# Kernel optimization log

Hardware: AMD Instinct MI355X
Metric: run time of the kernel (lower is better)

## Reference

```python
import jax, jax.numpy as jnp
import numpy as np
from jax import lax

B, L, D, H, OM = 16, 512, 2048, 512, 5


def _lstm(seq, wih, whh, bih, bhh):
    # seq: [T, B, F]; PyTorch gate order i, f, g, o
    Hh = whh.shape[1]
    Bb = seq.shape[1]
    def step(carry, xt):
        h, c = carry
        g = xt @ wih.T + h @ whh.T + bih + bhh
        i, f, gg, o = jnp.split(g, 4, axis=-1)
        c = jax.nn.sigmoid(f) * c + jax.nn.sigmoid(i) * jnp.tanh(gg)
        h = jax.nn.sigmoid(o) * jnp.tanh(c)
        return (h, c), h
    z = jnp.zeros((Bb, Hh), seq.dtype)
    _, hs = lax.scan(step, (z, z), seq)
    return hs  # [T, B, Hh]


def setup_inputs() -> dict:
    key = jax.random.key(0)
    ks = jax.random.split(key, 17)
    s = 0.02
    f32 = jnp.float32
    inp = {
        "x": jax.random.normal(ks[0], (B, L, D), f32),
        "wb": jax.random.normal(ks[1], (H, D, OM), f32) * s,
        "bb": jax.random.normal(ks[2], (H,), f32) * s,
        "wa": jax.random.normal(ks[3], (H, D, OM), f32) * s,
        "ba": jax.random.normal(ks[4], (H,), f32) * s,
        "wr": jax.random.normal(ks[5], (H, D, 2 * OM), f32) * s,
        "br": jax.random.normal(ks[6], (H,), f32) * s,
        "wih_f": jax.random.normal(ks[7], (4 * H, H + 1), f32) * s,
        "whh_f": jax.random.normal(ks[8], (4 * H, H), f32) * s,
        "bih_f": jax.random.normal(ks[9], (4 * H,), f32) * s,
        "bhh_f": jax.random.normal(ks[10], (4 * H,), f32) * s,
        "wih_r": jax.random.normal(ks[11], (4 * H, H + 1), f32) * s,
        "whh_r": jax.random.normal(ks[12], (4 * H, H), f32) * s,
        "bih_r": jax.random.normal(ks[13], (4 * H,), f32) * s,
        "bhh_r": jax.random.normal(ks[14], (4 * H,), f32) * s,
        "wfc": jax.random.normal(ks[15], (1, 2 * H), f32) * s,
        "bfc": jax.random.normal(ks[16], (1,), f32) * s,
    }
    return inp


def reference(x, wb, bb, wa, ba, wr, br, wih_f, whh_f, bih_f, bhh_f,
              wih_r, whh_r, bih_r, bhh_r, wfc, bfc):
    om = OM
    xc = jnp.transpose(x, (0, 2, 1))  # [B, D, L]
    conv = lambda w, b: lax.conv_general_dilated(
        xc, w, (1,), 'VALID', dimension_numbers=('NCH', 'OIH', 'NCH')) + b[None, :, None]
    cb = conv(wb, bb)  # [B, H, L-om+1]
    ca = conv(wa, ba)  # [B, H, L-om+1]
    cr = conv(wr, br)  # [B, H, L-2om+1]
    T = x.shape[1] - 2 * om  # number of centers c in [om, L-om)
    d_before = cb[:, :, 0:T]          # window [c-om, c) == conv output c-om
    d_after = ca[:, :, om:om + T]     # window [c, c+om) == conv output c
    vts_d = jnp.sum(d_before * d_after, axis=1, keepdims=True)  # [B, 1, T]
    vts_r = cr[:, :, 0:T]             # full window; pool over length-1 is identity
    vts_seq = jnp.concatenate([vts_r, vts_d], axis=1)  # [B, H+1, T]
    seq = jnp.transpose(vts_seq, (2, 0, 1))  # [T, B, H+1]
    hs_f = _lstm(seq, wih_f, whh_f, bih_f, bhh_f)
    hs_r = _lstm(seq[::-1], wih_r, whh_r, bih_r, bhh_r)[::-1]
    h = jnp.concatenate([hs_f, hs_r], axis=-1)  # [T, B, 2H]
    logits = jnp.einsum('tbh,h->tb', h, wfc[0]) + bfc[0]
    return jax.nn.sigmoid(jnp.transpose(logits))  # [B, T]
```

## Files before the change

### kernel.cpp

```cpp
#include <hip/hip_runtime.h>
#include <hip/hip_bf16.h>

typedef short v8s __attribute__((ext_vector_type(8)));
typedef float v4f __attribute__((ext_vector_type(4)));
typedef unsigned int u32;
typedef unsigned short u16;
typedef unsigned long long u64;

__device__ __forceinline__ u16 f2bf(float f) {
    union { float f; u32 u; } x; x.f = f;
    u32 r = x.u + 0x7fffu + ((x.u >> 16) & 1u);
    return (u16)(r >> 16);
}
__device__ __forceinline__ float bf2f(u16 s) {
    union { u32 u; float f; } x; x.u = ((u32)s) << 16;
    return x.f;
}
__device__ __forceinline__ float sigmoidf_(float x) { return 1.f / (1.f + __expf(-x)); }
__device__ __forceinline__ float tanh_fast(float x) {
    float t = fminf(fmaxf(x, -15.f), 15.f);
    float e = __expf(2.f * t);
    return (e - 1.f) / (e + 1.f);
}

__global__ __launch_bounds__(256) void xbf_kernel(const float* __restrict__ x, u16* __restrict__ xbf, int n) {
    int i = (blockIdx.x * 256 + threadIdx.x) * 4;
    if (i + 3 < n) {
        float4 v = *(const float4*)(x + i);
        u16* d = xbf + i;
        d[0] = f2bf(v.x); d[1] = f2bf(v.y); d[2] = f2bf(v.z); d[3] = f2bf(v.w);
    }
}

__global__ __launch_bounds__(256) void packw_kernel(const float* __restrict__ wb, const float* __restrict__ wa,
                                                    const float* __restrict__ wr, u16* __restrict__ W1, u16* __restrict__ W2) {
    long idx = (long)blockIdx.x * 256 + threadIdx.x;
    int which = idx >= (1024L * 10240) ? 1 : 0;
    long rem = idx - (long)which * 1024 * 10240;
    int n = (int)(rem / 10240);
    int kap = (int)(rem % 10240);
    int tap = kap >> 11, d = kap & 2047;
    float v;
    if (n < 512) v = which ? wa[(long)n * 10240 + d * 5 + tap] : wb[(long)n * 10240 + d * 5 + tap];
    else         v = wr[(long)(n - 512) * 20480 + d * 10 + tap + (which ? 5 : 0)];
    (which ? W2 : W1)[rem] = f2bf(v);
}

__global__ __launch_bounds__(256) void packwih_kernel(const float* __restrict__ wf, const float* __restrict__ wr,
                                                      u16* __restrict__ Bp) {
    int idx = blockIdx.x * 256 + threadIdx.x;
    int n = idx / 576, kap = idx % 576;
    int dir = n >> 11, g = n & 2047;
    const float* src = dir ? wr : wf;
    float v = (kap < 513) ? src[(long)g * 513 + kap] : 0.f;
    Bp[idx] = f2bf(v);
}

__global__ __launch_bounds__(256) void packwhh_kernel(const float* __restrict__ whf, const float* __restrict__ whr,
                                                      u16* __restrict__ W) {
    int idx = blockIdx.x * 256 + threadIdx.x;
    int dir = idx >> 20;
    float v = dir ? whr[idx & 1048575] : whf[idx];
    W[idx] = f2bf(v);
}

__global__ __launch_bounds__(256) void misc_kernel(const float* __restrict__ bihf, const float* __restrict__ bhhf,
                                                   const float* __restrict__ bihr, const float* __restrict__ bhhr,
                                                   float* __restrict__ bsum, u64* __restrict__ hbuf) {
    int i = blockIdx.x * 256 + threadIdx.x;
    if (i < 2048) bsum[i] = bihf[i] + bhhf[i];
    else if (i < 4096) bsum[i] = bihr[i - 2048] + bhhr[i - 2048];
    else if (i < 4096 + 16384) hbuf[i - 4096] = 0xFFFFFFFF00000000ULL;
}

template <int OUTBF>
__global__ __launch_bounds__(256) void gemm_bf16(const u16* __restrict__ A, const u16* __restrict__ B,
                                                 void* __restrict__ Cv, int M, int N, int K, int ldc,
                                                 int row_div, u32 row_mul1, u32 row_mul2, u32 row_base) {
    __shared__ u16 ldsA[128 * 64];
    __shared__ u16 ldsB[128 * 64];
    const int ntn = N >> 7;
    const int tm = blockIdx.x / ntn, tn = blockIdx.x % ntn;
    const int tid = threadIdx.x, lane = tid & 63, wv = tid >> 6;
    const int wm = wv >> 1, wn = wv & 1;
    const int qbase = wv * 4;

    u32 asrc[4], bsrc[4];
#pragma unroll
    for (int it = 0; it < 4; ++it) {
        int q = qbase + it;
        int r = q * 8 + (lane >> 3);
        int cb = ((lane & 7) * 16) ^ ((r & 7) << 4);
        int m = tm * 128 + r; if (m > M - 1) m = M - 1;
        asrc[it] = row_base + (u32)(m / row_div) * row_mul1 + (u32)(m % row_div) * row_mul2 + (u32)(cb >> 1);
        int n = tn * 128 + r;
        bsrc[it] = (u32)n * (u32)K + (u32)(cb >> 1);
    }

    v4f acc[4][4];
#pragma unroll
    for (int i = 0; i < 4; ++i)
#pragma unroll
        for (int j = 0; j < 4; ++j) acc[i][j] = (v4f){0.f, 0.f, 0.f, 0.f};

    const int KT = K >> 6;
    for (int kt = 0; kt < KT; ++kt) {
        const int k0 = kt << 6;
#pragma unroll
        for (int it = 0; it < 4; ++it) {
            int q = qbase + it;
            __builtin_amdgcn_global_load_lds(
                (const __attribute__((address_space(1))) u32*)(A + asrc[it] + k0),
                (__attribute__((address_space(3))) u32*)((char*)ldsA + q * 1024), 16, 0, 0);
            __builtin_amdgcn_global_load_lds(
                (const __attribute__((address_space(1))) u32*)(B + bsrc[it] + k0),
                (__attribute__((address_space(3))) u32*)((char*)ldsB + q * 1024), 16, 0, 0);
        }
        __syncthreads();
#pragma unroll
        for (int kk = 0; kk < 2; ++kk) {
            v8s af[4], bfr[4];
#pragma unroll
            for (int i = 0; i < 4; ++i) {
                int row = wm * 64 + i * 16 + (lane & 15);
                int cbyte = (kk * 64 + ((lane >> 4) * 16)) ^ ((row & 7) << 4);
                af[i] = *(const v8s*)((const char*)ldsA + row * 128 + cbyte);
                int rn = wn * 64 + i * 16 + (lane & 15);
                int cbn = (kk * 64 + ((lane >> 4) * 16)) ^ ((rn & 7) << 4);
                bfr[i] = *(const v8s*)((const char*)ldsB + rn * 128 + cbn);
            }
#pragma unroll
            for (int i = 0; i < 4; ++i)
#pragma unroll
                for (int j = 0; j < 4; ++j)
                    acc[i][j] = __builtin_amdgcn_mfma_f32_16x16x32_bf16(af[i], bfr[j], acc[i][j], 0, 0, 0);
        }
        __syncthreads();
    }
#pragma unroll
    for (int i = 0; i < 4; ++i)
#pragma unroll
        for (int j = 0; j < 4; ++j)
#pragma unroll
            for (int r = 0; r < 4; ++r) {
                int m = tm * 128 + wm * 64 + i * 16 + (lane >> 4) * 4 + r;
                int n = tn * 128 + wn * 64 + j * 16 + (lane & 15);
                if (m < M) {
                    if (OUTBF) ((u16*)Cv)[(long)m * ldc + n] = f2bf(acc[i][j][r]);
                    else       ((float*)Cv)[(long)m * ldc + n] = acc[i][j][r];
                }
            }
}

__global__ __launch_bounds__(256) void combine_kernel(const float* __restrict__ G1, const float* __restrict__ G2,
                                                      const float* __restrict__ bb, const float* __restrict__ ba,
                                                      const float* __restrict__ br, u16* __restrict__ seqpad) {
    int m = blockIdx.x;
    int b = m / 502, t = m % 502;
    int tid = threadIdx.x;
    const float* g1 = G1 + (long)m * 1024;
    const float* g2 = G2 + (long)m * 1024;
    u16* dst = seqpad + (long)(t * 16 + b) * 576;
    float part = 0.f;
#pragma unroll
    for (int rep = 0; rep < 2; ++rep) {
        int u = tid + rep * 256;
        float db = g1[u] + bb[u];
        float da = g2[u] + ba[u];
        part += db * da;
        float vr = g1[512 + u] + g2[512 + u] + br[u];
        dst[u] = f2bf(vr);
    }
#pragma unroll
    for (int off = 32; off; off >>= 1) part += __shfl_down(part, off, 64);
    __shared__ float red[4];
    if ((tid & 63) == 0) red[tid >> 6] = part;
    __syncthreads();
    if (tid == 0) dst[512] = f2bf(red[0] + red[1] + red[2] + red[3]);
    if (tid >= 1 && tid < 64) dst[512 + tid] = 0;
}

__global__ __launch_bounds__(256, 1) void lstm_kernel(const u16* __restrict__ P, const u16* __restrict__ whhbf,
                                                      const float* __restrict__ bsum, u64* hbuf,
                                                      u16* __restrict__ hs) {
    const int wg = blockIdx.x;
    const int dir = wg >> 4, j = wg & 15;
    const int tid = threadIdx.x, lane = tid & 63, w = tid >> 6;
    __shared__ u16 hls[16 * 512];
    __shared__ float gls[4][16][32];

    v8s bf[2][16];
    const u16* whd = whhbf + (long)dir * 2048 * 512;
#pragma unroll
    for (int nt = 0; nt < 2; ++nt) {
        int n = w * 512 + j * 32 + nt * 16 + (lane & 15);
#pragma unroll
        for (int kt = 0; kt < 16; ++kt)
            bf[nt][kt] = *(const v8s*)(whd + (long)n * 512 + kt * 32 + ((lane >> 4) * 8));
    }

    for (int i = tid; i < 8192; i += 256) hls[i] = 0;

    const int b_ = tid >> 4;
    const int u_ = (tid * 2) & 31;
    float c0 = 0.f, c1 = 0.f;
    u64* hb = hbuf + dir * 2 * 4096;

    const int col0 = w * 512 + j * 32 + (lane & 15);
    const float bs0 = bsum[dir * 2048 + col0];
    const float bs1 = bsum[dir * 2048 + col0 + 16];
    const u16* Pd = P + dir * 2048;

    float pv[2][4];
    {
        int tau = dir ? 501 : 0;
#pragma unroll
        for (int nt = 0; nt < 2; ++nt)
#pragma unroll
            for (int r = 0; r < 4; ++r) {
                int b = (lane >> 4) * 4 + r;
                pv[nt][r] = bf2f(Pd[(long)(tau * 16 + b) * 4096 + col0 + nt * 16]);
            }
    }
    __syncthreads();

    for (int s = 0; s < 502; ++s) {
        const int tau = dir ? (501 - s) : s;
        if (s > 0) {
            const u64* slot = hb + ((s - 1) & 1) * 4096;
            const u32 want = (u32)(s - 1);
            u64 vv[16];
            for (;;) {
                u32 ok = 0;
#pragma unroll
                for (int rep = 0; rep < 16; ++rep)
                    vv[rep] = __hip_atomic_load(slot + tid + rep * 256, __ATOMIC_RELAXED, __HIP_MEMORY_SCOPE_AGENT);
#pragma unroll
                for (int rep = 0; rep < 16; ++rep)
                    ok += ((u32)(vv[rep] >> 32) == want);
                if (ok == 16) break;
            }
#pragma unroll
            for (int rep = 0; rep < 16; ++rep) {
                int i = tid + rep * 256;
                int b = i >> 8;
                int byteoff = (b << 10) + (((i & 255) << 2) ^ ((b & 7) << 4));
                *(u32*)((char*)hls + byteoff) = (u32)vv[rep];
            }
            __syncthreads();
        }
        v4f acc[2];
#pragma unroll
        for (int nt = 0; nt < 2; ++nt)
#pragma unroll
            for (int r = 0; r < 4; ++r)
                acc[nt][r] = pv[nt][r] + (nt ? bs1 : bs0);
#pragma unroll
        for (int kt = 0; kt < 16; ++kt) {
            int row = lane & 15;
            int cbyte = (kt * 64 + ((lane >> 4) * 16)) ^ ((row & 7) << 4);
            v8s af = *(const v8s*)((const char*)hls + row * 1024 + cbyte);
            acc[0] = __builtin_amdgcn_mfma_f32_16x16x32_bf16(af, bf[0][kt], acc[0], 0, 0, 0);
            acc[1] = __builtin_amdgcn_mfma_f32_16x16x32_bf16(af, bf[1][kt], acc[1], 0, 0, 0);
        }
#pragma unroll
        for (int nt = 0; nt < 2; ++nt)
#pragma unroll
            for (int r = 0; r < 4; ++r)
                gls[w][(lane >> 4) * 4 + r][nt * 16 + (lane & 15)] = acc[nt][r];
        __syncthreads();

        float i0 = gls[0][b_][u_],     f0 = gls[1][b_][u_],     g0 = gls[2][b_][u_],     o0 = gls[3][b_][u_];
        float i1 = gls[0][b_][u_ + 1], f1 = gls[1][b_][u_ + 1], g1v = gls[2][b_][u_ + 1], o1 = gls[3][b_][u_ + 1];
        c0 = sigmoidf_(f0) * c0 + sigmoidf_(i0) * tanh_fast(g0);
        c1 = sigmoidf_(f1) * c1 + sigmoidf_(i1) * tanh_fast(g1v);
        float h0 = sigmoidf_(o0) * tanh_fast(c0);
        float h1 = sigmoidf_(o1) * tanh_fast(c1);
        u32 hw = (u32)f2bf(h0) | ((u32)f2bf(h1) << 16);
        int gi = (b_ * 512 + j * 32 + u_) >> 1;
        __hip_atomic_store(hb + (s & 1) * 4096 + gi, (u64)hw | ((u64)(u32)s << 32),
                           __ATOMIC_RELAXED, __HIP_MEMORY_SCOPE_AGENT);
        *(u32*)(hs + (((long)(dir * 502 + tau) * 16 + b_) * 512 + j * 32 + u_)) = hw;
        if (s + 1 < 502) {
            int tau2 = dir ? (500 - s) : (s + 1);
#pragma unroll
            for (int nt = 0; nt < 2; ++nt)
#pragma unroll
                for (int r = 0; r < 4; ++r) {
                    int b = (lane >> 4) * 4 + r;
                    pv[nt][r] = bf2f(Pd[(long)(tau2 * 16 + b) * 4096 + col0 + nt * 16]);
                }
        }
        __syncthreads();
    }
}

__global__ __launch_bounds__(256) void final_kernel(const u16* __restrict__ hs, const float* __restrict__ wfc,
                                                    const float* __restrict__ bfc, float* __restrict__ out) {
    int m = blockIdx.x;
    int t = m >> 4, b = m & 15;
    int tid = threadIdx.x;
    const u16* hf = hs + ((long)t * 16 + b) * 512;
    const u16* hr = hs + ((long)(502 + t) * 16 + b) * 512;
    float part = 0.f;
#pragma unroll
    for (int rep = 0; rep < 2; ++rep) {
        int u = tid + rep * 256;
        part += bf2f(hf[u]) * wfc[u] + bf2f(hr[u]) * wfc[512 + u];
    }
#pragma unroll
    for (int off = 32; off; off >>= 1) part += __shfl_down(part, off, 64);
    __shared__ float red[4];
    if ((tid & 63) == 0) red[tid >> 6] = part;
    __syncthreads();
    if (tid == 0) {
        float lg = red[0] + red[1] + red[2] + red[3] + bfc[0];
        out[(long)b * 502 + t] = 1.f / (1.f + __expf(-lg));
    }
}

extern "C" void kernel_launch(void* const* d_in, const int* in_sizes, int n_in,
                              void* d_out, int out_size, void* d_ws, size_t ws_size,
                              hipStream_t stream) {
    const float* x     = (const float*)d_in[0];
    const float* wb    = (const float*)d_in[1];
    const float* bb    = (const float*)d_in[2];
    const float* wa    = (const float*)d_in[3];
    const float* ba    = (const float*)d_in[4];
    const float* wr    = (const float*)d_in[5];
    const float* br    = (const float*)d_in[6];
    const float* wih_f = (const float*)d_in[7];
    const float* whh_f = (const float*)d_in[8];
    const float* bih_f = (const float*)d_in[9];
    const float* bhh_f = (const float*)d_in[10];
    const float* wih_r = (const float*)d_in[11];
    const float* whh_r = (const float*)d_in[12];
    const float* bih_r = (const float*)d_in[13];
    const float* bhh_r = (const float*)d_in[14];
    const float* wfc   = (const float*)d_in[15];
    const float* bfc   = (const float*)d_in[16];
    float* out = (float*)d_out;

    char* ws = (char*)d_ws;
    u16* xbf = (u16*)ws;
    u16* W1  = (u16*)(ws + 33554432);
    u16* W2  = (u16*)(ws + 54525952);
    u16* Pb  = (u16*)ws;
    char* r2 = ws + 75497472;
    float* G1 = (float*)r2;
    float* G2 = (float*)(r2 + 32899072);
    u16*  hs  = (u16*)r2;
    char* r3 = r2 + 65798144;
    u16*  seqp = (u16*)r3;
    u16*  wihp = (u16*)(r3 + 9252864);
    u16*  whhb = (u16*)(r3 + 13971456);
    float* bsum= (float*)(r3 + 18165760);
    u64*  hbuf = (u64*)(r3 + 18182144);

    xbf_kernel<<<16384, 256, 0, stream>>>(x, xbf, 16 * 512 * 2048);
    packw_kernel<<<81920, 256, 0, stream>>>(wb, wa, wr, W1, W2);
    packwih_kernel<<<9216, 256, 0, stream>>>(wih_f, wih_r, wihp);
    packwhh_kernel<<<8192, 256, 0, stream>>>(whh_f, whh_r, whhb);
    misc_kernel<<<80, 256, 0, stream>>>(bih_f, bhh_f, bih_r, bhh_r, bsum, hbuf);

    gemm_bf16<0><<<63 * 8, 256, 0, stream>>>(xbf, W1, G1, 8032, 1024, 10240, 1024,
                                             502, 512u * 2048u, 2048u, 0u);
    gemm_bf16<0><<<63 * 8, 256, 0, stream>>>(xbf, W2, G2, 8032, 1024, 10240, 1024,
                                             502, 512u * 2048u, 2048u, 5u * 2048u);
    combine_kernel<<<8032, 256, 0, stream>>>(G1, G2, bb, ba, br, seqp);
    gemm_bf16<1><<<63 * 32, 256, 0, stream>>>(seqp, wihp, Pb, 8032, 4096, 576, 4096,
                                              8032, 0u, 576u, 0u);
    lstm_kernel<<<32, 256, 0, stream>>>(Pb, whhb, bsum, hbuf, hs);
    final_kernel<<<8032, 256, 0, stream>>>(hs, wfc, bfc, out);
}
```

Baseline: 1.787 ms.

## Interleave forward and reverse LSTM directions in one workgroup to hide polling latency

```diff
diff --git a/kernel.cpp b/kernel.cpp
--- a/kernel.cpp
+++ b/kernel.cpp
@@ -183,116 +183,141 @@
 __global__ __launch_bounds__(256, 1) void lstm_kernel(const u16* __restrict__ P, const u16* __restrict__ whhbf,
                                                       const float* __restrict__ bsum, u64* hbuf,
                                                       u16* __restrict__ hs) {
-    const int wg = blockIdx.x;
-    const int dir = wg >> 4, j = wg & 15;
+    const int j = blockIdx.x;
     const int tid = threadIdx.x, lane = tid & 63, w = tid >> 6;
     __shared__ u16 hls[16 * 512];
     __shared__ float gls[4][16][32];
 
-    v8s bf[2][16];
-    const u16* whd = whhbf + (long)dir * 2048 * 512;
-#pragma unroll
-    for (int nt = 0; nt < 2; ++nt) {
-        int n = w * 512 + j * 32 + nt * 16 + (lane & 15);
-#pragma unroll
-        for (int kt = 0; kt < 16; ++kt)
-            bf[nt][kt] = *(const v8s*)(whd + (long)n * 512 + kt * 32 + ((lane >> 4) * 8));
-    }
-
+    v8s bf[2][2][16];
+#pragma unroll
+    for (int d = 0; d < 2; ++d) {
+        const u16* whd = whhbf + (long)d * 2048 * 512;
+#pragma unroll
+        for (int nt = 0; nt < 2; ++nt) {
+            int n = w * 512 + j * 32 + nt * 16 + (lane & 15);
+#pragma unroll
+            for (int kt = 0; kt < 16; ++kt)
+                bf[d][nt][kt] = *(const v8s*)(whd + (long)n * 512 + kt * 32 + ((lane >> 4) * 8));
+        }
+    }
     for (int i = tid; i < 8192; i += 256) hls[i] = 0;
 
     const int b_ = tid >> 4;
     const int u_ = (tid * 2) & 31;
-    float c0 = 0.f, c1 = 0.f;
-    u64* hb = hbuf + dir * 2 * 4096;
+    float cst[2][2] = {{0.f, 0.f}, {0.f, 0.f}};
+    u64* hb0 = hbuf;
+    u64* hb1 = hbuf + 2 * 4096;
 
     const int col0 = w * 512 + j * 32 + (lane & 15);
-    const float bs0 = bsum[dir * 2048 + col0];
-    const float bs1 = bsum[dir * 2048 + col0 + 16];
-    const u16* Pd = P + dir * 2048;
-
-    float pv[2][4];
-    {
-        int tau = dir ? 501 : 0;
+    float bs0[2], bs1[2];
+    bs0[0] = bsum[col0];        bs1[0] = bsum[col0 + 16];
+    bs0[1] = bsum[2048 + col0]; bs1[1] = bsum[2048 + col0 + 16];
+
+    float pv[2][2][4];
+#pragma unroll
+    for (int d = 0; d < 2; ++d) {
+        int tau = d ? 501 : 0;
+        const u16* Pd = P + d * 2048;
 #pragma unroll
         for (int nt = 0; nt < 2; ++nt)
 #pragma unroll
-            for (int r = 0; r < 4; ++r) {
-                int b = (lane >> 4) * 4 + r;
-                pv[nt][r] = bf2f(Pd[(long)(tau * 16 + b) * 4096 + col0 + nt * 16]);
-            }
-    }
+            for (int r = 0; r < 4; ++r)
+                pv[d][nt][r] = bf2f(Pd[(long)(tau * 16 + ((lane >> 4) * 4 + r)) * 4096 + col0 + nt * 16]);
+    }
+    u64 vv0[16], vv1[16];
     __syncthreads();
 
+#define POLL_ISSUE(slot, vv)                                                                        \
+    _Pragma("unroll")                                                                               \
+    for (int rep = 0; rep < 16; ++rep)                                                              \
+        vv[rep] = __hip_atomic_load((slot) + tid + rep * 256, __ATOMIC_RELAXED, __HIP_MEMORY_SCOPE_AGENT);
+
+#define POLL_FINISH_FILL(slot, want, vv)                                                            \
+    for (;;) {                                                                                      \
+        u32 ok = 0;                                                                                 \
+        _Pragma("unroll")                                                                           \
+        for (int rep = 0; rep < 16; ++rep) ok += ((u32)(vv[rep] >> 32) == (u32)(want));             \
+        if (ok == 16) break;                                                                        \
+        POLL_ISSUE(slot, vv)                                                                        \
+    }                                                                                               \
+    _Pragma("unroll")                                                                               \
+    for (int rep = 0; rep < 16; ++rep) {                                                            \
+        int i_ = tid + rep * 256;                                                                   \
+        int bb_ = i_ >> 8;                                                                          \
+        int bo_ = (bb_ << 10) + (((i_ & 255) << 2) ^ ((bb_ & 7) << 4));                             \
+        *(u32*)((char*)hls + bo_) = (u32)vv[rep];                                                   \
+    }
+
+#define MFMA_PHASE(d)                                                                               \
+    v4f a0a, a1a, a0b = (v4f){0, 0, 0, 0}, a1b = (v4f){0, 0, 0, 0};                                 \
+    _Pragma("unroll")                                                                               \
+    for (int r = 0; r < 4; ++r) { a0a[r] = pv[d][0][r] + bs0[d]; a1a[r] = pv[d][1][r] + bs1[d]; }   \
+    _Pragma("unroll")                                                                               \
+    for (int kt = 0; kt < 16; kt += 2) {                                                            \
+        int row = lane & 15;                                                                        \
+        int cb0 = (kt * 64 + ((lane >> 4) * 16)) ^ ((row & 7) << 4);                                \
+        int cb1 = ((kt + 1) * 64 + ((lane >> 4) * 16)) ^ ((row & 7) << 4);                          \
+        v8s af0 = *(const v8s*)((const char*)hls + row * 1024 + cb0);                               \
+        v8s af1 = *(const v8s*)((const char*)hls + row * 1024 + cb1);                               \
+        a0a = __builtin_amdgcn_mfma_f32_16x16x32_bf16(af0, bf[d][0][kt], a0a, 0, 0, 0);             \
+        a1a = __builtin_amdgcn_mfma_f32_16x16x32_bf16(af0, bf[d][1][kt], a1a, 0, 0, 0);             \
+        a0b = __builtin_amdgcn_mfma_f32_16x16x32_bf16(af1, bf[d][0][kt + 1], a0b, 0, 0, 0);         \
+        a1b = __builtin_amdgcn_mfma_f32_16x16x32_bf16(af1, bf[d][1][kt + 1], a1b, 0, 0, 0);         \
+    }                                                                                               \
+    _Pragma("unroll")                                                                               \
+    for (int r = 0; r < 4; ++r) {                                                                   \
+        gls[w][(lane >> 4) * 4 + r][(lane & 15)] = a0a[r] + a0b[r];                                 \
+        gls[w][(lane >> 4) * 4 + r][16 + (lane & 15)] = a1a[r] + a1b[r];                            \
+    }
+
+#define GATES_PHASE(d, hbd, s_, tau_)                                                               \
+    {                                                                                               \
+        float gi0 = gls[0][b_][u_],     gf0 = gls[1][b_][u_],     gg0 = gls[2][b_][u_],     go0 = gls[3][b_][u_];     \
+        float gi1 = gls[0][b_][u_ + 1], gf1 = gls[1][b_][u_ + 1], gg1 = gls[2][b_][u_ + 1], go1 = gls[3][b_][u_ + 1]; \
+        cst[d][0] = sigmoidf_(gf0) * cst[d][0] + sigmoidf_(gi0) * tanh_fast(gg0);                   \
+        cst[d][1] = sigmoidf_(gf1) * cst[d][1] + sigmoidf_(gi1) * tanh_fast(gg1);                   \
+        float h0 = sigmoidf_(go0) * tanh_fast(cst[d][0]);                                           \
+        float h1 = sigmoidf_(go1) * tanh_fast(cst[d][1]);                                           \
+        u32 hw = (u32)f2bf(h0) | ((u32)f2bf(h1) << 16);                                             \
+        int gi_ = (b_ * 512 + j * 32 + u_) >> 1;                                                    \
+        __hip_atomic_store(hbd + ((s_) & 1) * 4096 + gi_, (u64)hw | ((u64)(u32)(s_) << 32),         \
+                           __ATOMIC_RELAXED, __HIP_MEMORY_SCOPE_AGENT);                             \
+        *(u32*)(hs + (((long)((d) * 502 + (tau_)) * 16 + b_) * 512 + j * 32 + u_)) = hw;            \
+        if ((s_) + 1 < 502) {                                                                       \
+            int tau2 = (d) ? (500 - (s_)) : ((s_) + 1);                                             \
+            const u16* Pd = P + (d) * 2048;                                                         \
+            _Pragma("unroll")                                                                       \
+            for (int nt = 0; nt < 2; ++nt)                                                          \
+                _Pragma("unroll")                                                                   \
+                for (int r = 0; r < 4; ++r)                                                         \
+                    pv[d][nt][r] = bf2f(Pd[(long)(tau2 * 16 + ((lane >> 4) * 4 + r)) * 4096 + col0 + nt * 16]); \
+        }                                                                                           \
+    }
+
     for (int s = 0; s < 502; ++s) {
-        const int tau = dir ? (501 - s) : s;
         if (s > 0) {
-            const u64* slot = hb + ((s - 1) & 1) * 4096;
-            const u32 want = (u32)(s - 1);
-            u64 vv[16];
-            for (;;) {
-                u32 ok = 0;
-#pragma unroll
-                for (int rep = 0; rep < 16; ++rep)
-                    vv[rep] = __hip_atomic_load(slot + tid + rep * 256, __ATOMIC_RELAXED, __HIP_MEMORY_SCOPE_AGENT);
-#pragma unroll
-                for (int rep = 0; rep < 16; ++rep)
-                    ok += ((u32)(vv[rep] >> 32) == want);
-                if (ok == 16) break;
-            }
-#pragma unroll
-            for (int rep = 0; rep < 16; ++rep) {
-                int i = tid + rep * 256;
-                int b = i >> 8;
-                int byteoff = (b << 10) + (((i & 255) << 2) ^ ((b & 7) << 4));
-                *(u32*)((char*)hls + byteoff) = (u32)vv[rep];
-            }
-            __syncthreads();
+            u64* slot0 = hb0 + ((s - 1) & 1) * 4096;
+            POLL_FINISH_FILL(slot0, s - 1, vv0)
         }
-        v4f acc[2];
-#pragma unroll
-        for (int nt = 0; nt < 2; ++nt)
-#pragma unroll
-            for (int r = 0; r < 4; ++r)
-                acc[nt][r] = pv[nt][r] + (nt ? bs1 : bs0);
-#pragma unroll
-        for (int kt = 0; kt < 16; ++kt) {
-            int row = lane & 15;
-            int cbyte = (kt * 64 + ((lane >> 4) * 16)) ^ ((row & 7) << 4);
-            v8s af = *(const v8s*)((const char*)hls + row * 1024 + cbyte);
-            acc[0] = __builtin_amdgcn_mfma_f32_16x16x32_bf16(af, bf[0][kt], acc[0], 0, 0, 0);
-            acc[1] = __builtin_amdgcn_mfma_f32_16x16x32_bf16(af, bf[1][kt], acc[1], 0, 0, 0);
+        __syncthreads();
+        { MFMA_PHASE(0) }
+        __syncthreads();
+        if (s > 0) { u64* slot1 = hb1 + ((s - 1) & 1) * 4096; POLL_ISSUE(slot1, vv1) }
+        GATES_PHASE(0, hb0, s, s)
+        if (s > 0) {
+            u64* slot1 = hb1 + ((s - 1) & 1) * 4096;
+            POLL_FINISH_FILL(slot1, s - 1, vv1)
         }
-#pragma unroll
-        for (int nt = 0; nt < 2; ++nt)
-#pragma unroll
-            for (int r = 0; r < 4; ++r)
-                gls[w][(lane >> 4) * 4 + r][nt * 16 + (lane & 15)] = acc[nt][r];
-        __syncthreads();
-
-        float i0 = gls[0][b_][u_],     f0 = gls[1][b_][u_],     g0 = gls[2][b_][u_],     o0 = gls[3][b_][u_];
-        float i1 = gls[0][b_][u_ + 1], f1 = gls[1][b_][u_ + 1], g1v = gls[2][b_][u_ + 1], o1 = gls[3][b_][u_ + 1];
-        c0 = sigmoidf_(f0) * c0 + sigmoidf_(i0) * tanh_fast(g0);
-        c1 = sigmoidf_(f1) * c1 + sigmoidf_(i1) * tanh_fast(g1v);
-        float h0 = sigmoidf_(o0) * tanh_fast(c0);
-        float h1 = sigmoidf_(o1) * tanh_fast(c1);
-        u32 hw = (u32)f2bf(h0) | ((u32)f2bf(h1) << 16);
-        int gi = (b_ * 512 + j * 32 + u_) >> 1;
-        __hip_atomic_store(hb + (s & 1) * 4096 + gi, (u64)hw | ((u64)(u32)s << 32),
-                           __ATOMIC_RELAXED, __HIP_MEMORY_SCOPE_AGENT);
-        *(u32*)(hs + (((long)(dir * 502 + tau) * 16 + b_) * 512 + j * 32 + u_)) = hw;
-        if (s + 1 < 502) {
-            int tau2 = dir ? (500 - s) : (s + 1);
-#pragma unroll
-            for (int nt = 0; nt < 2; ++nt)
-#pragma unroll
-                for (int r = 0; r < 4; ++r) {
-                    int b = (lane >> 4) * 4 + r;
-                    pv[nt][r] = bf2f(Pd[(long)(tau2 * 16 + b) * 4096 + col0 + nt * 16]);
-                }
-        }
-        __syncthreads();
-    }
+        __syncthreads();
+        { MFMA_PHASE(1) }
+        __syncthreads();
+        if (s + 1 < 502) { u64* slot0 = hb0 + (s & 1) * 4096; POLL_ISSUE(slot0, vv0) }
+        GATES_PHASE(1, hb1, s, 501 - s)
+    }
+#undef POLL_ISSUE
+#undef POLL_FINISH_FILL
+#undef MFMA_PHASE
+#undef GATES_PHASE
 }
 
 __global__ __launch_bounds__(256) void final_kernel(const u16* __restrict__ hs, const float* __restrict__ wfc,
@@ -370,6 +395,6 @@
     combine_kernel<<<8032, 256, 0, stream>>>(G1, G2, bb, ba, br, seqp);
     gemm_bf16<1><<<63 * 32, 256, 0, stream>>>(seqp, wihp, Pb, 8032, 4096, 576, 4096,
                                               8032, 0u, 576u, 0u);
-    lstm_kernel<<<32, 256, 0, stream>>>(Pb, whhb, bsum, hbuf, hs);
+    lstm_kernel<<<16, 256, 0, stream>>>(Pb, whhb, bsum, hbuf, hs);
     final_kernel<<<8032, 256, 0, stream>>>(hs, wfc, bfc, out);
 }
```

New measurement: 3.051 ms. 1.71x slower.

## Replace per-element tagged h exchange with per-block flags and vector loads

Applied to the files above, without the earlier changes.

```diff
diff --git a/kernel.cpp b/kernel.cpp
--- a/kernel.cpp
+++ b/kernel.cpp
@@ -66,11 +66,11 @@
 
 __global__ __launch_bounds__(256) void misc_kernel(const float* __restrict__ bihf, const float* __restrict__ bhhf,
                                                    const float* __restrict__ bihr, const float* __restrict__ bhhr,
-                                                   float* __restrict__ bsum, u64* __restrict__ hbuf) {
+                                                   float* __restrict__ bsum, int* __restrict__ flags) {
     int i = blockIdx.x * 256 + threadIdx.x;
     if (i < 2048) bsum[i] = bihf[i] + bhhf[i];
     else if (i < 4096) bsum[i] = bihr[i - 2048] + bhhr[i - 2048];
-    else if (i < 4096 + 16384) hbuf[i - 4096] = 0xFFFFFFFF00000000ULL;
+    else if (i < 4096 + 32) flags[i - 4096] = -1;
 }
 
 template <int OUTBF>
@@ -181,7 +181,7 @@
 }
 
 __global__ __launch_bounds__(256, 1) void lstm_kernel(const u16* __restrict__ P, const u16* __restrict__ whhbf,
-                                                      const float* __restrict__ bsum, u64* hbuf,
+                                                      const float* __restrict__ bsum, u32* hdata, int* flags,
                                                       u16* __restrict__ hs) {
     const int wg = blockIdx.x;
     const int dir = wg >> 4, j = wg & 15;
@@ -204,72 +204,68 @@
     const int b_ = tid >> 4;
     const int u_ = (tid * 2) & 31;
     float c0 = 0.f, c1 = 0.f;
-    u64* hb = hbuf + dir * 2 * 4096;
+    u32* hd = hdata + dir * 2 * 4096;
+    int* fl = flags + dir * 16;
 
     const int col0 = w * 512 + j * 32 + (lane & 15);
     const float bs0 = bsum[dir * 2048 + col0];
     const float bs1 = bsum[dir * 2048 + col0 + 16];
     const u16* Pd = P + dir * 2048;
 
+    const int cj = tid >> 4;
+    const int cb = tid & 15;
+    const int rowbase = cb << 10;
+    const int xsw = (cb & 7) << 4;
+
     float pv[2][4];
     {
         int tau = dir ? 501 : 0;
 #pragma unroll
         for (int nt = 0; nt < 2; ++nt)
 #pragma unroll
-            for (int r = 0; r < 4; ++r) {
-                int b = (lane >> 4) * 4 + r;
-                pv[nt][r] = bf2f(Pd[(long)(tau * 16 + b) * 4096 + col0 + nt * 16]);
-            }
+            for (int r = 0; r < 4; ++r)
+                pv[nt][r] = bf2f(Pd[(long)(tau * 16 + ((lane >> 4) * 4 + r)) * 4096 + col0 + nt * 16]);
     }
     __syncthreads();
 
     for (int s = 0; s < 502; ++s) {
         const int tau = dir ? (501 - s) : s;
         if (s > 0) {
-            const u64* slot = hb + ((s - 1) & 1) * 4096;
-            const u32 want = (u32)(s - 1);
-            u64 vv[16];
-            for (;;) {
-                u32 ok = 0;
-#pragma unroll
-                for (int rep = 0; rep < 16; ++rep)
-                    vv[rep] = __hip_atomic_load(slot + tid + rep * 256, __ATOMIC_RELAXED, __HIP_MEMORY_SCOPE_AGENT);
-#pragma unroll
-                for (int rep = 0; rep < 16; ++rep)
-                    ok += ((u32)(vv[rep] >> 32) == want);
-                if (ok == 16) break;
-            }
-#pragma unroll
-            for (int rep = 0; rep < 16; ++rep) {
-                int i = tid + rep * 256;
-                int b = i >> 8;
-                int byteoff = (b << 10) + (((i & 255) << 2) ^ ((b & 7) << 4));
-                *(u32*)((char*)hls + byteoff) = (u32)vv[rep];
-            }
-            __syncthreads();
-        }
-        v4f acc[2];
-#pragma unroll
-        for (int nt = 0; nt < 2; ++nt)
-#pragma unroll
-            for (int r = 0; r < 4; ++r)
-                acc[nt][r] = pv[nt][r] + (nt ? bs1 : bs0);
-#pragma unroll
-        for (int kt = 0; kt < 16; ++kt) {
+            const int want = s - 1;
+            int fv;
+            do {
+                fv = __hip_atomic_load(fl + (lane & 15), __ATOMIC_RELAXED, __HIP_MEMORY_SCOPE_AGENT);
+            } while (!__all(fv >= want));
+            __builtin_amdgcn_fence(__ATOMIC_ACQUIRE, "agent");
+            const uint4* src = (const uint4*)(hd + ((s - 1) & 1) * 4096) + tid * 4;
+            uint4 d0 = src[0], d1 = src[1], d2 = src[2], d3 = src[3];
+            *(uint4*)((char*)hls + rowbase + ((cj * 64 +  0) ^ xsw)) = d0;
+            *(uint4*)((char*)hls + rowbase + ((cj * 64 + 16) ^ xsw)) = d1;
+            *(uint4*)((char*)hls + rowbase + ((cj * 64 + 32) ^ xsw)) = d2;
+            *(uint4*)((char*)hls + rowbase + ((cj * 64 + 48) ^ xsw)) = d3;
+        }
+        __syncthreads();
+        v4f a0a, a1a, a0b = (v4f){0, 0, 0, 0}, a1b = (v4f){0, 0, 0, 0};
+#pragma unroll
+        for (int r = 0; r < 4; ++r) { a0a[r] = pv[0][r] + bs0; a1a[r] = pv[1][r] + bs1; }
+#pragma unroll
+        for (int kt = 0; kt < 16; kt += 2) {
             int row = lane & 15;
-            int cbyte = (kt * 64 + ((lane >> 4) * 16)) ^ ((row & 7) << 4);
-            v8s af = *(const v8s*)((const char*)hls + row * 1024 + cbyte);
-            acc[0] = __builtin_amdgcn_mfma_f32_16x16x32_bf16(af, bf[0][kt], acc[0], 0, 0, 0);
-            acc[1] = __builtin_amdgcn_mfma_f32_16x16x32_bf16(af, bf[1][kt], acc[1], 0, 0, 0);
-        }
-#pragma unroll
-        for (int nt = 0; nt < 2; ++nt)
-#pragma unroll
-            for (int r = 0; r < 4; ++r)
-                gls[w][(lane >> 4) * 4 + r][nt * 16 + (lane & 15)] = acc[nt][r];
-        __syncthreads();
-
+            int cb0 = (kt * 64 + ((lane >> 4) * 16)) ^ ((row & 7) << 4);
+            int cb1 = ((kt + 1) * 64 + ((lane >> 4) * 16)) ^ ((row & 7) << 4);
+            v8s af0 = *(const v8s*)((const char*)hls + row * 1024 + cb0);
+            v8s af1 = *(const v8s*)((const char*)hls + row * 1024 + cb1);
+            a0a = __builtin_amdgcn_mfma_f32_16x16x32_bf16(af0, bf[0][kt], a0a, 0, 0, 0);
+            a1a = __builtin_amdgcn_mfma_f32_16x16x32_bf16(af0, bf[1][kt], a1a, 0, 0, 0);
+            a0b = __builtin_amdgcn_mfma_f32_16x16x32_bf16(af1, bf[0][kt + 1], a0b, 0, 0, 0);
+            a1b = __builtin_amdgcn_mfma_f32_16x16x32_bf16(af1, bf[1][kt + 1], a1b, 0, 0, 0);
+        }
+#pragma unroll
+        for (int r = 0; r < 4; ++r) {
+            gls[w][(lane >> 4) * 4 + r][(lane & 15)] = a0a[r] + a0b[r];
+            gls[w][(lane >> 4) * 4 + r][16 + (lane & 15)] = a1a[r] + a1b[r];
+        }
+        __syncthreads();
         float i0 = gls[0][b_][u_],     f0 = gls[1][b_][u_],     g0 = gls[2][b_][u_],     o0 = gls[3][b_][u_];
         float i1 = gls[0][b_][u_ + 1], f1 = gls[1][b_][u_ + 1], g1v = gls[2][b_][u_ + 1], o1 = gls[3][b_][u_ + 1];
         c0 = sigmoidf_(f0) * c0 + sigmoidf_(i0) * tanh_fast(g0);
@@ -277,21 +273,19 @@
         float h0 = sigmoidf_(o0) * tanh_fast(c0);
         float h1 = sigmoidf_(o1) * tanh_fast(c1);
         u32 hw = (u32)f2bf(h0) | ((u32)f2bf(h1) << 16);
-        int gi = (b_ * 512 + j * 32 + u_) >> 1;
-        __hip_atomic_store(hb + (s & 1) * 4096 + gi, (u64)hw | ((u64)(u32)s << 32),
-                           __ATOMIC_RELAXED, __HIP_MEMORY_SCOPE_AGENT);
+        hd[(s & 1) * 4096 + j * 256 + tid] = hw;
         *(u32*)(hs + (((long)(dir * 502 + tau) * 16 + b_) * 512 + j * 32 + u_)) = hw;
         if (s + 1 < 502) {
             int tau2 = dir ? (500 - s) : (s + 1);
 #pragma unroll
             for (int nt = 0; nt < 2; ++nt)
 #pragma unroll
-                for (int r = 0; r < 4; ++r) {
-                    int b = (lane >> 4) * 4 + r;
-                    pv[nt][r] = bf2f(Pd[(long)(tau2 * 16 + b) * 4096 + col0 + nt * 16]);
-                }
-        }
-        __syncthreads();
+                for (int r = 0; r < 4; ++r)
+                    pv[nt][r] = bf2f(Pd[(long)(tau2 * 16 + ((lane >> 4) * 4 + r)) * 4096 + col0 + nt * 16]);
+        }
+        __syncthreads();
+        if (tid == 0)
+            __hip_atomic_store(fl + j, s, __ATOMIC_RELEASE, __HIP_MEMORY_SCOPE_AGENT);
     }
 }
 
@@ -355,13 +349,14 @@
     u16*  wihp = (u16*)(r3 + 9252864);
     u16*  whhb = (u16*)(r3 + 13971456);
     float* bsum= (float*)(r3 + 18165760);
-    u64*  hbuf = (u64*)(r3 + 18182144);
+    u32*  hdata= (u32*) (r3 + 18182144);
+    int*  flags= (int*) (r3 + 18247680);
 
     xbf_kernel<<<16384, 256, 0, stream>>>(x, xbf, 16 * 512 * 2048);
     packw_kernel<<<81920, 256, 0, stream>>>(wb, wa, wr, W1, W2);
     packwih_kernel<<<9216, 256, 0, stream>>>(wih_f, wih_r, wihp);
     packwhh_kernel<<<8192, 256, 0, stream>>>(whh_f, whh_r, whhb);
-    misc_kernel<<<80, 256, 0, stream>>>(bih_f, bhh_f, bih_r, bhh_r, bsum, hbuf);
+    misc_kernel<<<17, 256, 0, stream>>>(bih_f, bhh_f, bih_r, bhh_r, bsum, flags);
 
     gemm_bf16<0><<<63 * 8, 256, 0, stream>>>(xbf, W1, G1, 8032, 1024, 10240, 1024,
                                              502, 512u * 2048u, 2048u, 0u);
@@ -370,6 +365,6 @@
     combine_kernel<<<8032, 256, 0, stream>>>(G1, G2, bb, ba, br, seqp);
     gemm_bf16<1><<<63 * 32, 256, 0, stream>>>(seqp, wihp, Pb, 8032, 4096, 576, 4096,
                                               8032, 0u, 576u, 0u);
-    lstm_kernel<<<32, 256, 0, stream>>>(Pb, whhb, bsum, hbuf, hs);
+    lstm_kernel<<<32, 256, 0, stream>>>(Pb, whhb, bsum, hdata, flags, hs);
     final_kernel<<<8032, 256, 0, stream>>>(hs, wfc, bfc, out);
 }
```

After: 3.087 ms. 72.8% more time.
